# Kernel tuning notes

Measured on AMD Instinct MI355X. Metric: run time of the kernel, lower is better.

Reference implementation:

```python
import jax, jax.numpy as jnp
import numpy as np

D_MODEL = 1024
N_HEADS = 16
DEPTH = D_MODEL // N_HEADS
B, S = 2, 2048


def setup_inputs() -> dict:
    key = jax.random.key(0)
    ks = jax.random.split(key, 11)
    scale = 1.0 / np.sqrt(D_MODEL)
    return {
        "q": jax.random.normal(ks[0], (B, S, D_MODEL), jnp.float32),
        "k": jax.random.normal(ks[1], (B, S, D_MODEL), jnp.float32),
        "v": jax.random.normal(ks[2], (B, S, D_MODEL), jnp.float32),
        "wq": jax.random.normal(ks[3], (D_MODEL, D_MODEL), jnp.float32) * scale,
        "bq": jnp.zeros((D_MODEL,), jnp.float32),
        "wk": jax.random.normal(ks[4], (D_MODEL, D_MODEL), jnp.float32) * scale,
        "bk": jnp.zeros((D_MODEL,), jnp.float32),
        "wv": jax.random.normal(ks[5], (D_MODEL, D_MODEL), jnp.float32) * scale,
        "bv": jnp.zeros((D_MODEL,), jnp.float32),
        "wo": jax.random.normal(ks[6], (D_MODEL, D_MODEL), jnp.float32) * scale,
        "bo": jnp.zeros((D_MODEL,), jnp.float32),
    }


def _mha(q, k, v, wq, bq, wk, bk, wv, bv, wo, bo):
    b, s, _ = q.shape
    # separate QKV projections
    qh = (q @ wq + bq).reshape(b, s, N_HEADS, DEPTH).transpose(0, 2, 1, 3)  # [b,h,s,d]
    kh = (k @ wk + bk).reshape(b, s, N_HEADS, DEPTH).transpose(0, 2, 1, 3)
    vh = (v @ wv + bv).reshape(b, s, N_HEADS, DEPTH).transpose(0, 2, 1, 3)
    # keras.layers.Attention default: UNSCALED dot-product scores, causal mask
    scores = jnp.einsum("bhqd,bhkd->bhqk", qh, kh)  # [b,h,s,s]
    causal = jnp.tril(jnp.ones((s, s), bool))
    scores = jnp.where(causal, scores, jnp.float32(-1e9))
    attn = jax.nn.softmax(scores, axis=-1)
    out = jnp.einsum("bhqk,bhkd->bhqd", attn, vh)  # [b,h,s,d]
    out = out.transpose(0, 2, 1, 3).reshape(b, s, D_MODEL)
    return out @ wo + bo


def reference(q, k, v, wq, bq, wk, bk, wv, bv, wo, bo):
    return _mha(q, k, v, wq, bq, wk, bk, wv, bv, wo, bo)
```

## Files before the change

### kernel.cpp

```cpp
#include <hip/hip_runtime.h>
#include <stdint.h>

#define AS1q __attribute__((address_space(1)))
#define AS3q __attribute__((address_space(3)))

typedef unsigned short US;
typedef __bf16 bf16x8 __attribute__((ext_vector_type(8)));
typedef float f32x4 __attribute__((ext_vector_type(4)));

__device__ __forceinline__ US f2bf(float f) {
  union { float f; uint32_t u; } c; c.f = f;
  uint32_t u = c.u;
  return (US)((u + 0x7fffu + ((u >> 16) & 1u)) >> 16);
}

__device__ __forceinline__ float bf2f(US h) {
  union { uint32_t u; float f; } c; c.u = ((uint32_t)h) << 16; return c.f;
}

__device__ __forceinline__ bf16x8 asb(uint4 u) {
  union { uint4 u; bf16x8 b; } c; c.u = u; return c.b;
}

__device__ __forceinline__ void gload16(const void* g, void* l) {
  __builtin_amdgcn_global_load_lds((AS1q void*)(void*)g, (AS3q void*)l, 16, 0, 0);
}

__global__ void cvt3_kernel(const float* __restrict__ q, const float* __restrict__ k,
                            const float* __restrict__ v,
                            US* __restrict__ qb, US* __restrict__ kb, US* __restrict__ vb) {
  const float* s; US* d;
  if (blockIdx.y == 0)      { s = q; d = qb; }
  else if (blockIdx.y == 1) { s = k; d = kb; }
  else                      { s = v; d = vb; }
  int i = (blockIdx.x * 256 + threadIdx.x) * 8;
  float4 f0 = *(const float4*)&s[i];
  float4 f1 = *(const float4*)&s[i + 4];
  ushort4 u0, u1;
  u0.x = f2bf(f0.x); u0.y = f2bf(f0.y); u0.z = f2bf(f0.z); u0.w = f2bf(f0.w);
  u1.x = f2bf(f1.x); u1.y = f2bf(f1.y); u1.z = f2bf(f1.z); u1.w = f2bf(f1.w);
  *(ushort4*)&d[i] = u0;
  *(ushort4*)&d[i + 4] = u1;
}

__global__ void wtrans4_kernel(const float* __restrict__ w0, const float* __restrict__ w1,
                               const float* __restrict__ w2, const float* __restrict__ w3,
                               US* __restrict__ t0, US* __restrict__ t1,
                               US* __restrict__ t2, US* __restrict__ t3) {
  const float* W; US* Wt;
  if (blockIdx.z == 0)      { W = w0; Wt = t0; }
  else if (blockIdx.z == 1) { W = w1; Wt = t1; }
  else if (blockIdx.z == 2) { W = w2; Wt = t2; }
  else                      { W = w3; Wt = t3; }
  __shared__ US T[64 * 68];
  const int k0 = blockIdx.y * 64, n0 = blockIdx.x * 64;
  const int t = threadIdx.x;
#pragma unroll
  for (int it = 0; it < 4; ++it) {
    int q = t + it * 256;
    int row = q >> 4, c4 = (q & 15) * 4;
    float4 f = *(const float4*)&W[(k0 + row) * 1024 + n0 + c4];
    ushort4 u;
    u.x = f2bf(f.x); u.y = f2bf(f.y); u.z = f2bf(f.z); u.w = f2bf(f.w);
    *(ushort4*)&T[row * 68 + c4] = u;
  }
  __syncthreads();
#pragma unroll
  for (int it = 0; it < 4; ++it) {
    int q = t + it * 256;
    int rn = q >> 4, ck = (q & 15) * 4;
    ushort4 o;
    o.x = T[(ck + 0) * 68 + rn];
    o.y = T[(ck + 1) * 68 + rn];
    o.z = T[(ck + 2) * 68 + rn];
    o.w = T[(ck + 3) * 68 + rn];
    *(ushort4*)&Wt[(n0 + rn) * 1024 + k0 + ck] = o;
  }
}

__device__ __forceinline__ void gemm_core(const US* A, const US* Wt,
                                          int m0, int n0, US* As, US* Bs,
                                          f32x4 acc[4][4]) {
  const int tid = threadIdx.x;
  const int wave = tid >> 6, lane = tid & 63;
  const int quad = lane >> 4, l16 = lane & 15;
  const int wm = wave >> 1, wn = wave & 1;
#pragma unroll
  for (int i = 0; i < 4; ++i)
#pragma unroll
    for (int j = 0; j < 4; ++j) acc[i][j] = (f32x4)0.0f;
  const int p = wave * 64 + lane;
  const int arow0 = p >> 2, koff = (p & 3) * 8;
  for (int k0 = 0; k0 < 1024; k0 += 32) {
    gload16(A + (m0 + arow0) * 1024 + k0 + koff, As + wave * 512);
    gload16(A + (m0 + arow0 + 64) * 1024 + k0 + koff, As + 2048 + wave * 512);
    gload16(Wt + (n0 + arow0) * 1024 + k0 + koff, Bs + wave * 512);
    gload16(Wt + (n0 + arow0 + 64) * 1024 + k0 + koff, Bs + 2048 + wave * 512);
    __syncthreads();
    uint4 af[4], bf_[4];
#pragma unroll
    for (int mt = 0; mt < 4; ++mt)
      af[mt] = *(const uint4*)&As[(wm * 64 + mt * 16 + l16) * 32 + quad * 8];
#pragma unroll
    for (int nt = 0; nt < 4; ++nt)
      bf_[nt] = *(const uint4*)&Bs[(wn * 64 + nt * 16 + l16) * 32 + quad * 8];
#pragma unroll
    for (int mt = 0; mt < 4; ++mt)
#pragma unroll
      for (int nt = 0; nt < 4; ++nt)
        acc[mt][nt] = __builtin_amdgcn_mfma_f32_16x16x32_bf16(asb(af[mt]), asb(bf_[nt]),
                                                              acc[mt][nt], 0, 0, 0);
    __syncthreads();
  }
}

__global__ __launch_bounds__(256, 2) void gemm_qkv_kernel(
    const US* __restrict__ qb, const US* __restrict__ kb, const US* __restrict__ vb,
    const US* __restrict__ wqT, const US* __restrict__ wkT, const US* __restrict__ wvT,
    const float* __restrict__ bq, const float* __restrict__ bk, const float* __restrict__ bv,
    US* __restrict__ qh, US* __restrict__ kh, US* __restrict__ vt) {
  __shared__ __align__(16) US As[4096], Bs[4096];
  const US* A; const US* W; const float* bias;
  if (blockIdx.z == 0)      { A = qb; W = wqT; bias = bq; }
  else if (blockIdx.z == 1) { A = kb; W = wkT; bias = bk; }
  else                      { A = vb; W = wvT; bias = bv; }
  const int m0 = blockIdx.y * 128, n0 = blockIdx.x * 128;
  f32x4 acc[4][4];
  gemm_core(A, W, m0, n0, As, Bs, acc);
  const int tid = threadIdx.x, wave = tid >> 6, lane = tid & 63;
  const int quad = lane >> 4, l16 = lane & 15;
  const int wm = wave >> 1, wn = wave & 1;
  if (blockIdx.z == 2) {
#pragma unroll
    for (int nt = 0; nt < 4; ++nt) {
      int n = n0 + wn * 64 + nt * 16 + l16;
      float bval = bias[n];
      int hh = n >> 6, d = n & 63;
#pragma unroll
      for (int mt = 0; mt < 4; ++mt) {
        int m = m0 + wm * 64 + mt * 16 + quad * 4;
        int bb = m >> 11, s = m & 2047;
        ushort4 u;
        u.x = f2bf(acc[mt][nt][0] + bval);
        u.y = f2bf(acc[mt][nt][1] + bval);
        u.z = f2bf(acc[mt][nt][2] + bval);
        u.w = f2bf(acc[mt][nt][3] + bval);
        *(ushort4*)&vt[((bb * 16 + hh) * 64 + d) * 2048 + s] = u;
      }
    }
  } else {
    US* O = (blockIdx.z == 0) ? qh : kh;
#pragma unroll
    for (int nt = 0; nt < 4; ++nt) {
      int n = n0 + wn * 64 + nt * 16 + l16;
      float bval = bias[n];
      int hh = n >> 6, d = n & 63;
#pragma unroll
      for (int mt = 0; mt < 4; ++mt) {
#pragma unroll
        for (int r = 0; r < 4; ++r) {
          int m = m0 + wm * 64 + mt * 16 + quad * 4 + r;
          int bb = m >> 11, s = m & 2047;
          O[((bb * 16 + hh) * 2048 + s) * 64 + d] = f2bf(acc[mt][nt][r] + bval);
        }
      }
    }
  }
}

__global__ __launch_bounds__(256, 2) void gemm_out_kernel(
    const US* __restrict__ ao, const US* __restrict__ woT,
    const float* __restrict__ bo, float* __restrict__ out) {
  __shared__ __align__(16) US As[4096], Bs[4096];
  const int m0 = blockIdx.y * 128, n0 = blockIdx.x * 128;
  f32x4 acc[4][4];
  gemm_core(ao, woT, m0, n0, As, Bs, acc);
  const int tid = threadIdx.x, wave = tid >> 6, lane = tid & 63;
  const int quad = lane >> 4, l16 = lane & 15;
  const int wm = wave >> 1, wn = wave & 1;
#pragma unroll
  for (int nt = 0; nt < 4; ++nt) {
    int n = n0 + wn * 64 + nt * 16 + l16;
    float bval = bo[n];
#pragma unroll
    for (int mt = 0; mt < 4; ++mt) {
#pragma unroll
      for (int r = 0; r < 4; ++r) {
        int m = m0 + wm * 64 + mt * 16 + quad * 4 + r;
        out[m * 1024 + n] = acc[mt][nt][r] + bval;
      }
    }
  }
}

__global__ __launch_bounds__(256, 2) void attn_kernel(
    const US* __restrict__ qh, const US* __restrict__ kh,
    const US* __restrict__ vt, US* __restrict__ aout) {
  __shared__ __align__(16) US Qs[4096];
  __shared__ __align__(16) US Ks[2][4096];
  __shared__ __align__(16) US Vs[2][4096];
  __shared__ __align__(16) US Ps[4608];
  const int tid = threadIdx.x;
  const int wave = tid >> 6, lane = tid & 63;
  const int quad = lane >> 4, l16 = lane & 15;
  const int bh = blockIdx.y;
  const int b = bh >> 4, h = bh & 15;
  const int pair = blockIdx.x;

  const int pp0 = wave * 64 + lane;
  const int row0 = pp0 >> 3, c0 = (pp0 & 7) ^ (row0 & 7);
  const int pp1 = 256 + pp0;
  const int row1 = pp1 >> 3, c1 = (pp1 & 7) ^ (row1 & 7);

  const US* gkb = kh + (size_t)bh * 2048 * 64;
  const US* gvb = vt + (size_t)bh * 64 * 2048;

  for (int half = 0; half < 2; ++half) {
    const int qt = half ? (31 - pair) : pair;
    const int q0 = qt * 64;
    __syncthreads();
    {
      const US* gq = qh + ((size_t)bh * 2048 + q0) * 64;
      gload16(gq + row0 * 64 + c0 * 8, Qs + wave * 512);
      gload16(gq + row1 * 64 + c1 * 8, Qs + 2048 + wave * 512);
      gload16(gkb + row0 * 64 + c0 * 8, Ks[0] + wave * 512);
      gload16(gkb + row1 * 64 + c1 * 8, Ks[0] + 2048 + wave * 512);
      gload16(gvb + row0 * 2048 + c0 * 8, Vs[0] + wave * 512);
      gload16(gvb + row1 * 2048 + c1 * 8, Vs[0] + 2048 + wave * 512);
    }
    __syncthreads();

    const int qrow = wave * 16 + l16;
    uint4 aq0 = *(const uint4*)&Qs[qrow * 64 + ((quad ^ (qrow & 7)) * 8)];
    uint4 aq1 = *(const uint4*)&Qs[qrow * 64 + (((4 + quad) ^ (qrow & 7)) * 8)];

    float l_part[4] = {0.f, 0.f, 0.f, 0.f};
    f32x4 Of[4];
#pragma unroll
    for (int nt = 0; nt < 4; ++nt) Of[nt] = (f32x4)0.0f;
    const int grow_base = q0 + wave * 16 + quad * 4;

    for (int kt = 0; kt <= qt; ++kt) {
      const int cb = kt & 1;
      if (kt) __syncthreads();
      if (kt < qt) {
        US* kd = Ks[cb ^ 1];
        US* vd = Vs[cb ^ 1];
        const US* gk = gkb + (kt + 1) * 64 * 64;
        const US* gv = gvb + (kt + 1) * 64;
        gload16(gk + row0 * 64 + c0 * 8, kd + wave * 512);
        gload16(gk + row1 * 64 + c1 * 8, kd + 2048 + wave * 512);
        gload16(gv + row0 * 2048 + c0 * 8, vd + wave * 512);
        gload16(gv + row1 * 2048 + c1 * 8, vd + 2048 + wave * 512);
      }
      const US* Kc = Ks[cb];
      const US* Vc = Vs[cb];

      f32x4 sacc[4];
#pragma unroll
      for (int nt = 0; nt < 4; ++nt) sacc[nt] = (f32x4)0.0f;
#pragma unroll
      for (int nt = 0; nt < 4; ++nt) {
        int krow = nt * 16 + l16;
        uint4 bk0 = *(const uint4*)&Kc[krow * 64 + ((quad ^ (krow & 7)) * 8)];
        sacc[nt] = __builtin_amdgcn_mfma_f32_16x16x32_bf16(asb(aq0), asb(bk0), sacc[nt], 0, 0, 0);
      }
#pragma unroll
      for (int nt = 0; nt < 4; ++nt) {
        int krow = nt * 16 + l16;
        uint4 bk1 = *(const uint4*)&Kc[krow * 64 + (((4 + quad) ^ (krow & 7)) * 8)];
        sacc[nt] = __builtin_amdgcn_mfma_f32_16x16x32_bf16(asb(aq1), asb(bk1), sacc[nt], 0, 0, 0);
      }
      if (kt == qt) {
#pragma unroll
        for (int nt = 0; nt < 4; ++nt) {
          int gcol = q0 + nt * 16 + l16;
#pragma unroll
          for (int r = 0; r < 4; ++r)
            if (gcol > grow_base + r) sacc[nt][r] = -1e30f;
        }
      }

      US* pw = Ps + wave * 16 * 72;
#pragma unroll
      for (int nt = 0; nt < 4; ++nt) {
#pragma unroll
        for (int r = 0; r < 4; ++r) {
          float e = __expf(sacc[nt][r]);
          US hb = f2bf(e);
          l_part[r] += bf2f(hb);
          pw[(quad * 4 + r) * 72 + nt * 16 + l16] = hb;
        }
      }
      __asm__ volatile("s_waitcnt lgkmcnt(0)" ::: "memory");

#pragma unroll
      for (int ks = 0; ks < 2; ++ks) {
        uint4 ap = *(const uint4*)&pw[l16 * 72 + ks * 32 + quad * 8];
#pragma unroll
        for (int nt = 0; nt < 4; ++nt) {
          int vrow = nt * 16 + l16;
          uint4 bv_ = *(const uint4*)&Vc[vrow * 64 + (((ks * 4 + quad) ^ (vrow & 7)) * 8)];
          Of[nt] = __builtin_amdgcn_mfma_f32_16x16x32_bf16(asb(ap), asb(bv_), Of[nt], 0, 0, 0);
        }
      }
    }

#pragma unroll
    for (int r = 0; r < 4; ++r) {
      float s = l_part[r];
#pragma unroll
      for (int off = 1; off < 16; off <<= 1) s += __shfl_xor(s, off, 64);
      float inv = 1.0f / s;
      int srow = grow_base + r;
#pragma unroll
      for (int nt = 0; nt < 4; ++nt)
        aout[((size_t)b * 2048 + srow) * 1024 + h * 64 + nt * 16 + l16] = f2bf(Of[nt][r] * inv);
    }
  }
}

extern "C" void kernel_launch(void* const* d_in, const int* in_sizes, int n_in,
                              void* d_out, int out_size, void* d_ws, size_t ws_size,
                              hipStream_t stream) {
  const float* q  = (const float*)d_in[0];
  const float* k  = (const float*)d_in[1];
  const float* v  = (const float*)d_in[2];
  const float* wq = (const float*)d_in[3];
  const float* bq = (const float*)d_in[4];
  const float* wk = (const float*)d_in[5];
  const float* bk = (const float*)d_in[6];
  const float* wv = (const float*)d_in[7];
  const float* bv = (const float*)d_in[8];
  const float* wo = (const float*)d_in[9];
  const float* bo = (const float*)d_in[10];
  float* out = (float*)d_out;

  char* ws = (char*)d_ws;
  const size_t MB = 1024 * 1024;
  US* qb  = (US*)(ws + 0 * MB);
  US* kb  = (US*)(ws + 8 * MB);
  US* vb  = (US*)(ws + 16 * MB);
  US* wqT = (US*)(ws + 24 * MB);
  US* wkT = (US*)(ws + 26 * MB);
  US* wvT = (US*)(ws + 28 * MB);
  US* woT = (US*)(ws + 30 * MB);
  US* qh  = (US*)(ws + 32 * MB);
  US* kh  = (US*)(ws + 40 * MB);
  US* vt  = (US*)(ws + 48 * MB);
  US* ao  = (US*)(ws + 56 * MB);

  cvt3_kernel<<<dim3(2048, 3), 256, 0, stream>>>(q, k, v, qb, kb, vb);
  wtrans4_kernel<<<dim3(16, 16, 4), 256, 0, stream>>>(wq, wk, wv, wo, wqT, wkT, wvT, woT);
  gemm_qkv_kernel<<<dim3(8, 32, 3), 256, 0, stream>>>(qb, kb, vb, wqT, wkT, wvT,
                                                      bq, bk, bv, qh, kh, vt);
  attn_kernel<<<dim3(16, 32), 256, 0, stream>>>(qh, kh, vt, ao);
  gemm_out_kernel<<<dim3(8, 32), 256, 0, stream>>>(ao, woT, bo, out);
}
```

Measured before the change: 230.8 us.

## Split attention KV tile across 8 waves, fuse prep kernels, swap GEMM grid order

The attention kernel goes to 512 threads. Each pair of waves shares a 16-row query slice and splits the 64-key tile in half, and the partial O and l sums are combined through shared memory at the end. The fp32-to-bf16 conversion and weight-transpose kernels are merged into one launch to cut a kernel launch. The GEMM and attention grids swap x/y so consecutive blocks walk M (or heads) first, which changes L2 reuse of weights. The cost is extra LDS for the reduction and two more barriers per query tile.

```diff
diff --git a/kernel.cpp b/kernel.cpp
--- a/kernel.cpp
+++ b/kernel.cpp
@@ -26,39 +26,44 @@
   __builtin_amdgcn_global_load_lds((AS1q void*)(void*)g, (AS3q void*)l, 16, 0, 0);
 }
 
-__global__ void cvt3_kernel(const float* __restrict__ q, const float* __restrict__ k,
+__global__ void prep_kernel(const float* __restrict__ q, const float* __restrict__ k,
                             const float* __restrict__ v,
-                            US* __restrict__ qb, US* __restrict__ kb, US* __restrict__ vb) {
-  const float* s; US* d;
-  if (blockIdx.y == 0)      { s = q; d = qb; }
-  else if (blockIdx.y == 1) { s = k; d = kb; }
-  else                      { s = v; d = vb; }
-  int i = (blockIdx.x * 256 + threadIdx.x) * 8;
-  float4 f0 = *(const float4*)&s[i];
-  float4 f1 = *(const float4*)&s[i + 4];
-  ushort4 u0, u1;
-  u0.x = f2bf(f0.x); u0.y = f2bf(f0.y); u0.z = f2bf(f0.z); u0.w = f2bf(f0.w);
-  u1.x = f2bf(f1.x); u1.y = f2bf(f1.y); u1.z = f2bf(f1.z); u1.w = f2bf(f1.w);
-  *(ushort4*)&d[i] = u0;
-  *(ushort4*)&d[i + 4] = u1;
-}
-
-__global__ void wtrans4_kernel(const float* __restrict__ w0, const float* __restrict__ w1,
-                               const float* __restrict__ w2, const float* __restrict__ w3,
-                               US* __restrict__ t0, US* __restrict__ t1,
-                               US* __restrict__ t2, US* __restrict__ t3) {
+                            const float* __restrict__ w0, const float* __restrict__ w1,
+                            const float* __restrict__ w2, const float* __restrict__ w3,
+                            US* __restrict__ qb, US* __restrict__ kb, US* __restrict__ vb,
+                            US* __restrict__ t0, US* __restrict__ t1,
+                            US* __restrict__ t2, US* __restrict__ t3) {
+  __shared__ US T[64 * 68];
+  const int bx = blockIdx.x;
+  const int t = threadIdx.x;
+  if (bx < 6144) {
+    const int ten = bx >> 11, chunk = bx & 2047;
+    const float* s; US* d;
+    if (ten == 0)      { s = q; d = qb; }
+    else if (ten == 1) { s = k; d = kb; }
+    else               { s = v; d = vb; }
+    int i = (chunk * 256 + t) * 8;
+    float4 f0 = *(const float4*)&s[i];
+    float4 f1 = *(const float4*)&s[i + 4];
+    ushort4 u0, u1;
+    u0.x = f2bf(f0.x); u0.y = f2bf(f0.y); u0.z = f2bf(f0.z); u0.w = f2bf(f0.w);
+    u1.x = f2bf(f1.x); u1.y = f2bf(f1.y); u1.z = f2bf(f1.z); u1.w = f2bf(f1.w);
+    *(ushort4*)&d[i] = u0;
+    *(ushort4*)&d[i + 4] = u1;
+    return;
+  }
+  const int idx = bx - 6144;
+  const int wsel = idx >> 8, rem = idx & 255;
+  const int n0 = (rem & 15) * 64, k0 = (rem >> 4) * 64;
   const float* W; US* Wt;
-  if (blockIdx.z == 0)      { W = w0; Wt = t0; }
-  else if (blockIdx.z == 1) { W = w1; Wt = t1; }
-  else if (blockIdx.z == 2) { W = w2; Wt = t2; }
-  else                      { W = w3; Wt = t3; }
-  __shared__ US T[64 * 68];
-  const int k0 = blockIdx.y * 64, n0 = blockIdx.x * 64;
-  const int t = threadIdx.x;
+  if (wsel == 0)      { W = w0; Wt = t0; }
+  else if (wsel == 1) { W = w1; Wt = t1; }
+  else if (wsel == 2) { W = w2; Wt = t2; }
+  else                { W = w3; Wt = t3; }
 #pragma unroll
   for (int it = 0; it < 4; ++it) {
-    int q = t + it * 256;
-    int row = q >> 4, c4 = (q & 15) * 4;
+    int p = t + it * 256;
+    int row = p >> 4, c4 = (p & 15) * 4;
     float4 f = *(const float4*)&W[(k0 + row) * 1024 + n0 + c4];
     ushort4 u;
     u.x = f2bf(f.x); u.y = f2bf(f.y); u.z = f2bf(f.z); u.w = f2bf(f.w);
@@ -67,8 +72,8 @@
   __syncthreads();
 #pragma unroll
   for (int it = 0; it < 4; ++it) {
-    int q = t + it * 256;
-    int rn = q >> 4, ck = (q & 15) * 4;
+    int p = t + it * 256;
+    int rn = p >> 4, ck = (p & 15) * 4;
     ushort4 o;
     o.x = T[(ck + 0) * 68 + rn];
     o.y = T[(ck + 1) * 68 + rn];
@@ -124,7 +129,7 @@
   if (blockIdx.z == 0)      { A = qb; W = wqT; bias = bq; }
   else if (blockIdx.z == 1) { A = kb; W = wkT; bias = bk; }
   else                      { A = vb; W = wvT; bias = bv; }
-  const int m0 = blockIdx.y * 128, n0 = blockIdx.x * 128;
+  const int m0 = blockIdx.x * 128, n0 = blockIdx.y * 128;
   f32x4 acc[4][4];
   gemm_core(A, W, m0, n0, As, Bs, acc);
   const int tid = threadIdx.x, wave = tid >> 6, lane = tid & 63;
@@ -172,7 +177,7 @@
     const US* __restrict__ ao, const US* __restrict__ woT,
     const float* __restrict__ bo, float* __restrict__ out) {
   __shared__ __align__(16) US As[4096], Bs[4096];
-  const int m0 = blockIdx.y * 128, n0 = blockIdx.x * 128;
+  const int m0 = blockIdx.x * 128, n0 = blockIdx.y * 128;
   f32x4 acc[4][4];
   gemm_core(ao, woT, m0, n0, As, Bs, acc);
   const int tid = threadIdx.x, wave = tid >> 6, lane = tid & 63;
@@ -193,24 +198,24 @@
   }
 }
 
-__global__ __launch_bounds__(256, 2) void attn_kernel(
+__global__ __launch_bounds__(512, 4) void attn_kernel(
     const US* __restrict__ qh, const US* __restrict__ kh,
     const US* __restrict__ vt, US* __restrict__ aout) {
   __shared__ __align__(16) US Qs[4096];
   __shared__ __align__(16) US Ks[2][4096];
   __shared__ __align__(16) US Vs[2][4096];
-  __shared__ __align__(16) US Ps[4608];
+  __shared__ __align__(16) US Ps[8 * 640];
+  __shared__ float Oex[4][16][68];
+  __shared__ float lEx[4][16];
   const int tid = threadIdx.x;
   const int wave = tid >> 6, lane = tid & 63;
   const int quad = lane >> 4, l16 = lane & 15;
-  const int bh = blockIdx.y;
+  const int w_m = wave & 3, w_k = wave >> 2;
+  const int bh = blockIdx.x;
   const int b = bh >> 4, h = bh & 15;
-  const int pair = blockIdx.x;
-
-  const int pp0 = wave * 64 + lane;
-  const int row0 = pp0 >> 3, c0 = (pp0 & 7) ^ (row0 & 7);
-  const int pp1 = 256 + pp0;
-  const int row1 = pp1 >> 3, c1 = (pp1 & 7) ^ (row1 & 7);
+  const int pair = blockIdx.y;
+
+  const int srow = tid >> 3, sc = (tid & 7) ^ (srow & 7);
 
   const US* gkb = kh + (size_t)bh * 2048 * 64;
   const US* gvb = vt + (size_t)bh * 64 * 2048;
@@ -221,101 +226,115 @@
     __syncthreads();
     {
       const US* gq = qh + ((size_t)bh * 2048 + q0) * 64;
-      gload16(gq + row0 * 64 + c0 * 8, Qs + wave * 512);
-      gload16(gq + row1 * 64 + c1 * 8, Qs + 2048 + wave * 512);
-      gload16(gkb + row0 * 64 + c0 * 8, Ks[0] + wave * 512);
-      gload16(gkb + row1 * 64 + c1 * 8, Ks[0] + 2048 + wave * 512);
-      gload16(gvb + row0 * 2048 + c0 * 8, Vs[0] + wave * 512);
-      gload16(gvb + row1 * 2048 + c1 * 8, Vs[0] + 2048 + wave * 512);
-    }
-    __syncthreads();
-
-    const int qrow = wave * 16 + l16;
-    uint4 aq0 = *(const uint4*)&Qs[qrow * 64 + ((quad ^ (qrow & 7)) * 8)];
-    uint4 aq1 = *(const uint4*)&Qs[qrow * 64 + (((4 + quad) ^ (qrow & 7)) * 8)];
+      gload16(gq + srow * 64 + sc * 8, Qs + wave * 512);
+      gload16(gkb + srow * 64 + sc * 8, Ks[0] + wave * 512);
+      gload16(gvb + srow * 2048 + sc * 8, Vs[0] + wave * 512);
+    }
+    __syncthreads();
+
+    const int qrow = w_m * 16 + l16;
+    uint4 aq0 = *(const uint4*)&Qs[qrow * 64 + (((0 * 4 + quad) ^ (qrow & 7)) * 8)];
+    uint4 aq1 = *(const uint4*)&Qs[qrow * 64 + (((1 * 4 + quad) ^ (qrow & 7)) * 8)];
 
     float l_part[4] = {0.f, 0.f, 0.f, 0.f};
     f32x4 Of[4];
 #pragma unroll
     for (int nt = 0; nt < 4; ++nt) Of[nt] = (f32x4)0.0f;
-    const int grow_base = q0 + wave * 16 + quad * 4;
+    const int grow_base = q0 + w_m * 16 + quad * 4;
+
+    US* pw = Ps + wave * 640;
 
     for (int kt = 0; kt <= qt; ++kt) {
       const int cb = kt & 1;
       if (kt) __syncthreads();
       if (kt < qt) {
-        US* kd = Ks[cb ^ 1];
-        US* vd = Vs[cb ^ 1];
         const US* gk = gkb + (kt + 1) * 64 * 64;
         const US* gv = gvb + (kt + 1) * 64;
-        gload16(gk + row0 * 64 + c0 * 8, kd + wave * 512);
-        gload16(gk + row1 * 64 + c1 * 8, kd + 2048 + wave * 512);
-        gload16(gv + row0 * 2048 + c0 * 8, vd + wave * 512);
-        gload16(gv + row1 * 2048 + c1 * 8, vd + 2048 + wave * 512);
+        gload16(gk + srow * 64 + sc * 8, Ks[cb ^ 1] + wave * 512);
+        gload16(gv + srow * 2048 + sc * 8, Vs[cb ^ 1] + wave * 512);
       }
       const US* Kc = Ks[cb];
       const US* Vc = Vs[cb];
 
-      f32x4 sacc[4];
-#pragma unroll
-      for (int nt = 0; nt < 4; ++nt) sacc[nt] = (f32x4)0.0f;
-#pragma unroll
-      for (int nt = 0; nt < 4; ++nt) {
-        int krow = nt * 16 + l16;
+      f32x4 sacc[2];
+      sacc[0] = (f32x4)0.0f; sacc[1] = (f32x4)0.0f;
+#pragma unroll
+      for (int nt = 0; nt < 2; ++nt) {
+        int krow = w_k * 32 + nt * 16 + l16;
         uint4 bk0 = *(const uint4*)&Kc[krow * 64 + ((quad ^ (krow & 7)) * 8)];
         sacc[nt] = __builtin_amdgcn_mfma_f32_16x16x32_bf16(asb(aq0), asb(bk0), sacc[nt], 0, 0, 0);
       }
 #pragma unroll
-      for (int nt = 0; nt < 4; ++nt) {
-        int krow = nt * 16 + l16;
+      for (int nt = 0; nt < 2; ++nt) {
+        int krow = w_k * 32 + nt * 16 + l16;
         uint4 bk1 = *(const uint4*)&Kc[krow * 64 + (((4 + quad) ^ (krow & 7)) * 8)];
         sacc[nt] = __builtin_amdgcn_mfma_f32_16x16x32_bf16(asb(aq1), asb(bk1), sacc[nt], 0, 0, 0);
       }
       if (kt == qt) {
 #pragma unroll
-        for (int nt = 0; nt < 4; ++nt) {
-          int gcol = q0 + nt * 16 + l16;
+        for (int nt = 0; nt < 2; ++nt) {
+          int gcol = q0 + w_k * 32 + nt * 16 + l16;
 #pragma unroll
           for (int r = 0; r < 4; ++r)
             if (gcol > grow_base + r) sacc[nt][r] = -1e30f;
         }
       }
 
-      US* pw = Ps + wave * 16 * 72;
-#pragma unroll
-      for (int nt = 0; nt < 4; ++nt) {
+#pragma unroll
+      for (int nt = 0; nt < 2; ++nt) {
 #pragma unroll
         for (int r = 0; r < 4; ++r) {
           float e = __expf(sacc[nt][r]);
           US hb = f2bf(e);
           l_part[r] += bf2f(hb);
-          pw[(quad * 4 + r) * 72 + nt * 16 + l16] = hb;
+          pw[(quad * 4 + r) * 40 + nt * 16 + l16] = hb;
         }
       }
       __asm__ volatile("s_waitcnt lgkmcnt(0)" ::: "memory");
 
-#pragma unroll
-      for (int ks = 0; ks < 2; ++ks) {
-        uint4 ap = *(const uint4*)&pw[l16 * 72 + ks * 32 + quad * 8];
-#pragma unroll
-        for (int nt = 0; nt < 4; ++nt) {
-          int vrow = nt * 16 + l16;
-          uint4 bv_ = *(const uint4*)&Vc[vrow * 64 + (((ks * 4 + quad) ^ (vrow & 7)) * 8)];
-          Of[nt] = __builtin_amdgcn_mfma_f32_16x16x32_bf16(asb(ap), asb(bv_), Of[nt], 0, 0, 0);
-        }
-      }
-    }
-
+      uint4 ap = *(const uint4*)&pw[l16 * 40 + quad * 8];
+#pragma unroll
+      for (int nt = 0; nt < 4; ++nt) {
+        int vrow = nt * 16 + l16;
+        uint4 bv_ = *(const uint4*)&Vc[vrow * 64 + (((w_k * 4 + quad) ^ (vrow & 7)) * 8)];
+        Of[nt] = __builtin_amdgcn_mfma_f32_16x16x32_bf16(asb(ap), asb(bv_), Of[nt], 0, 0, 0);
+      }
+    }
+
+    float l_red[4];
 #pragma unroll
     for (int r = 0; r < 4; ++r) {
       float s = l_part[r];
 #pragma unroll
       for (int off = 1; off < 16; off <<= 1) s += __shfl_xor(s, off, 64);
-      float inv = 1.0f / s;
-      int srow = grow_base + r;
+      l_red[r] = s;
+    }
+
+    __syncthreads();
+    if (w_k == 1) {
 #pragma unroll
       for (int nt = 0; nt < 4; ++nt)
-        aout[((size_t)b * 2048 + srow) * 1024 + h * 64 + nt * 16 + l16] = f2bf(Of[nt][r] * inv);
+#pragma unroll
+        for (int r = 0; r < 4; ++r)
+          Oex[w_m][quad * 4 + r][nt * 16 + l16] = Of[nt][r];
+      if (l16 == 0) {
+#pragma unroll
+        for (int r = 0; r < 4; ++r) lEx[w_m][quad * 4 + r] = l_red[r];
+      }
+    }
+    __syncthreads();
+    if (w_k == 0) {
+#pragma unroll
+      for (int r = 0; r < 4; ++r) {
+        float ltot = l_red[r] + lEx[w_m][quad * 4 + r];
+        float inv = 1.0f / ltot;
+        int row = grow_base + r;
+#pragma unroll
+        for (int nt = 0; nt < 4; ++nt) {
+          float o = Of[nt][r] + Oex[w_m][quad * 4 + r][nt * 16 + l16];
+          aout[((size_t)b * 2048 + row) * 1024 + h * 64 + nt * 16 + l16] = f2bf(o * inv);
+        }
+      }
     }
   }
 }
@@ -350,10 +369,10 @@
   US* vt  = (US*)(ws + 48 * MB);
   US* ao  = (US*)(ws + 56 * MB);
 
-  cvt3_kernel<<<dim3(2048, 3), 256, 0, stream>>>(q, k, v, qb, kb, vb);
-  wtrans4_kernel<<<dim3(16, 16, 4), 256, 0, stream>>>(wq, wk, wv, wo, wqT, wkT, wvT, woT);
-  gemm_qkv_kernel<<<dim3(8, 32, 3), 256, 0, stream>>>(qb, kb, vb, wqT, wkT, wvT,
+  prep_kernel<<<7168, 256, 0, stream>>>(q, k, v, wq, wk, wv, wo,
+                                        qb, kb, vb, wqT, wkT, wvT, woT);
+  gemm_qkv_kernel<<<dim3(32, 8, 3), 256, 0, stream>>>(qb, kb, vb, wqT, wkT, wvT,
                                                       bq, bk, bv, qh, kh, vt);
-  attn_kernel<<<dim3(16, 32), 256, 0, stream>>>(qh, kh, vt, ao);
-  gemm_out_kernel<<<dim3(8, 32), 256, 0, stream>>>(ao, woT, bo, out);
-}
+  attn_kernel<<<dim3(32, 16), 512, 0, stream>>>(qh, kh, vt, ao);
+  gemm_out_kernel<<<dim3(32, 8), 256, 0, stream>>>(ao, woT, bo, out);
+}
```

Result: faster. 219.7 us (-4.8%).
